# Kernel optimization log

Hardware: AMD Instinct MI355X
Metric: run time of the kernel (lower is better)

Reference implementation:

```python
import jax, jax.numpy as jnp
import numpy as np
import math

H_HEADS, N_LEVELS, N_POINTS, DIM = 8, 4, 4, 256
HEAD_DIM = DIM // H_HEADS
SHAPES = np.array([[150, 150], [75, 75], [38, 38], [19, 19]], dtype=np.int32)
LEVEL_START = np.concatenate([[0], np.cumsum(SHAPES[:, 0] * SHAPES[:, 1])[:-1]]).astype(np.int32)
NUM_VALUE = int((SHAPES[:, 0] * SHAPES[:, 1]).sum())  # 29930
BS, NQ = 4, 22500


def _offset_bias():
    # Deformable-DETR init: points arranged on rays per head
    thetas = np.arange(H_HEADS, dtype=np.float32) * (2.0 * math.pi / H_HEADS)
    grid = np.stack([np.cos(thetas), np.sin(thetas)], -1)
    grid = grid / np.abs(grid).max(-1, keepdims=True)
    grid = np.tile(grid[:, None, None, :], (1, N_LEVELS, N_POINTS, 1))
    grid = grid * (np.arange(N_POINTS, dtype=np.float32) + 1.0)[None, None, :, None]
    return jnp.asarray(grid.reshape(-1))


def setup_inputs() -> dict:
    key = jax.random.key(0)
    ks = jax.random.split(key, 8)
    xav = lambda k, fi, fo: jax.random.normal(k, (fi, fo), jnp.float32) * np.float32(math.sqrt(2.0 / (fi + fo)))
    return {
        "query": jax.random.normal(ks[0], (BS, NQ, DIM), jnp.float32),
        "value": jax.random.normal(ks[1], (BS, NUM_VALUE, DIM), jnp.float32),
        "reference_points": jax.random.uniform(ks[2], (BS, NQ, N_LEVELS, 2), jnp.float32),
        "spatial_shapes": jnp.asarray(SHAPES),
        "level_start_index": jnp.asarray(LEVEL_START),
        "W_so": xav(ks[3], DIM, H_HEADS * N_LEVELS * N_POINTS * 2) * 0.1,
        "b_so": _offset_bias(),
        "W_aw": xav(ks[4], DIM, H_HEADS * N_LEVELS * N_POINTS) * 0.1,
        "b_aw": jnp.zeros((H_HEADS * N_LEVELS * N_POINTS,), jnp.float32),
        "W_v": xav(ks[5], DIM, DIM),
        "b_v": jnp.zeros((DIM,), jnp.float32),
        "W_o": xav(ks[6], DIM, DIM),
        "b_o": jnp.zeros((DIM,), jnp.float32),
    }


def _sample_level(v_l, loc_l, h, w):
    # v_l: (bs, H, h*w, hd); loc_l: (bs, nq, H, P, 2) in [0,1] normalized coords
    # torch grid_sample bilinear, align_corners=False, padding_mode='zeros'
    bs, nq = loc_l.shape[0], loc_l.shape[1]
    x = jnp.transpose(loc_l[..., 0], (0, 2, 1, 3)).reshape(bs, H_HEADS, nq * N_POINTS) * w - 0.5
    y = jnp.transpose(loc_l[..., 1], (0, 2, 1, 3)).reshape(bs, H_HEADS, nq * N_POINTS) * h - 0.5
    x0 = jnp.floor(x); y0 = jnp.floor(y)
    lx = x - x0; ly = y - y0

    def gather(xi, yi, wgt):
        valid = ((xi >= 0) & (xi < w) & (yi >= 0) & (yi < h)).astype(v_l.dtype)
        idx = (jnp.clip(yi, 0, h - 1) * w + jnp.clip(xi, 0, w - 1)).astype(jnp.int32)
        g = jnp.take_along_axis(v_l, idx[..., None], axis=2)  # (bs,H,nq*P,hd)
        return g * (wgt * valid)[..., None]

    x0i = x0.astype(jnp.int32); y0i = y0.astype(jnp.int32)
    out = (gather(x0i, y0i, (1 - lx) * (1 - ly))
           + gather(x0i + 1, y0i, lx * (1 - ly))
           + gather(x0i, y0i + 1, (1 - lx) * ly)
           + gather(x0i + 1, y0i + 1, lx * ly))
    return out.reshape(bs, H_HEADS, nq, N_POINTS, HEAD_DIM)


def reference(query, value, reference_points, spatial_shapes, level_start_index,
              W_so, b_so, W_aw, b_aw, W_v, b_v, W_o, b_o):
    shapes = np.asarray(jax.device_get(spatial_shapes))  # static level shapes
    starts = np.asarray(jax.device_get(level_start_index))
    bs, nq, _ = query.shape
    nv = value.shape[1]

    v = (value @ W_v + b_v).reshape(bs, nv, H_HEADS, HEAD_DIM)
    v = jnp.transpose(v, (0, 2, 1, 3))  # (bs, H, nv, hd)

    off = (query @ W_so + b_so).reshape(bs, nq, H_HEADS, N_LEVELS, N_POINTS, 2)
    aw = jax.nn.softmax((query @ W_aw + b_aw).reshape(bs, nq, H_HEADS, N_LEVELS * N_POINTS), axis=-1)
    aw = aw.reshape(bs, nq, H_HEADS, N_LEVELS, N_POINTS)

    norm = jnp.asarray(np.stack([shapes[:, 1], shapes[:, 0]], -1), query.dtype)  # (L, 2) = (W, H)
    loc = reference_points[:, :, None, :, None, :] + off / norm[None, None, None, :, None, :]

    res = jnp.zeros((bs, nq, H_HEADS, HEAD_DIM), query.dtype)
    for lvl in range(N_LEVELS):
        h, w = int(shapes[lvl, 0]), int(shapes[lvl, 1])
        s = int(starts[lvl])
        v_l = v[:, :, s:s + h * w, :]
        sampled = _sample_level(v_l, loc[:, :, :, lvl], h, w)  # (bs,H,nq,P,hd)
        res = res + jnp.einsum('bhqpd,bqhp->bqhd', sampled, aw[:, :, :, lvl])

    out = res.reshape(bs, nq, DIM) @ W_o + b_o
    return out  # dropout is identity in eval mode
```

## Files before the change

### kernel.cpp

```cpp
#include <hip/hip_runtime.h>
#include <hip/hip_bf16.h>

#define HH 8
#define NL 4
#define NP 4
#define DDIM 256
#define HD 32
#define BSZ 4
#define NQQ 22500
#define NVV 29930

typedef __attribute__((ext_vector_type(4))) float f32x4;
typedef __attribute__((ext_vector_type(8))) short s16x8;

__device__ __forceinline__ float bf16bits2float(unsigned short u) {
    union { unsigned int i; float f; } x;
    x.i = ((unsigned int)u) << 16;
    return x.f;
}
__device__ __forceinline__ unsigned short bfb(float x) {
    union { float f; unsigned int i; } u; u.f = x;
    unsigned int lsb = (u.i >> 16) & 1u;
    u.i += 0x7fffu + lsb;
    return (unsigned short)(u.i >> 16);
}
__device__ __forceinline__ s16x8 cvt8(float4 a, float4 b) {
    s16x8 r;
    r[0] = (short)bfb(a.x); r[1] = (short)bfb(a.y);
    r[2] = (short)bfb(a.z); r[3] = (short)bfb(a.w);
    r[4] = (short)bfb(b.x); r[5] = (short)bfb(b.y);
    r[6] = (short)bfb(b.z); r[7] = (short)bfb(b.w);
    return r;
}

__global__ __launch_bounds__(64) void k_pack(
    const float* __restrict__ Wso, const float* __restrict__ Waw,
    const float* __restrict__ Wv,  const float* __restrict__ Wo,
    unsigned short* __restrict__ pWv, unsigned short* __restrict__ pQP,
    unsigned short* __restrict__ pWo)
{
    const int ctg = blockIdx.x;
    const int lane = threadIdx.x;
    const float* src; unsigned short* dst; int N, col, ct;
    if (ctg < 16)      { ct = ctg;      dst = pWv; src = Wv; N = 256; col = ct*16 + (lane&15); }
    else if (ctg < 40) { ct = ctg - 16; dst = pQP;
        if (ct < 16) { src = Wso; N = 256; col = ct*16 + (lane&15); }
        else         { src = Waw; N = 128; col = (ct-16)*16 + (lane&15); } }
    else               { ct = ctg - 40; dst = pWo; src = Wo; N = 256; col = ct*16 + (lane&15); }

    for (int ks = 0; ks < 8; ++ks) {
        const int k0 = ks*32 + (lane>>4)*8;
        unsigned short tmp[8];
#pragma unroll
        for (int i = 0; i < 8; ++i) tmp[i] = bfb(src[(size_t)(k0 + i) * N + col]);
        unsigned short* d = dst + ((size_t)(ct*8 + ks)*64 + lane)*8;
#pragma unroll
        for (int i = 0; i < 8; ++i) d[i] = tmp[i];
    }
}

__global__ __launch_bounds__(256) void k_value_proj(
    const float* __restrict__ value,
    const float* __restrict__ bv,
    const unsigned short* __restrict__ pWv,
    unsigned short* __restrict__ vout)
{
    const int tid = threadIdx.x;
    const int b   = blockIdx.y;
    const int row0 = blockIdx.x * 64;
    const int w = tid >> 6, lane = tid & 63;
    const int mrow = lane & 15, kg = lane >> 4;

    const int rowa = row0 + w*16 + mrow;
    const bool rv = rowa < NVV;
    const float* ap = value + ((size_t)b * NVV + (rv ? rowa : 0)) * DDIM + kg*8;

    s16x8 af[8];
#pragma unroll
    for (int ks = 0; ks < 8; ++ks) {
        float4 a0 = make_float4(0.f,0.f,0.f,0.f), a1 = a0;
        if (rv) { a0 = *(const float4*)(ap + ks*32); a1 = *(const float4*)(ap + ks*32 + 4); }
        af[ks] = cvt8(a0, a1);
    }
    const s16x8* bp = (const s16x8*)pWv;
#pragma unroll 2
    for (int ct = 0; ct < 16; ++ct) {
        const float bias = bv[ct*16 + mrow];
        f32x4 acc = {bias, bias, bias, bias};
#pragma unroll
        for (int ks = 0; ks < 8; ++ks)
            acc = __builtin_amdgcn_mfma_f32_16x16x32_bf16(af[ks], bp[(ct*8 + ks)*64 + lane], acc, 0, 0, 0);
        const int h = ct >> 1, d = (ct & 1)*16 + mrow;
        unsigned short* vp = vout + ((size_t)(b*HH + h) * NVV) * HD + d;
#pragma unroll
        for (int r = 0; r < 4; ++r) {
            const int rowd = row0 + w*16 + kg*4 + r;
            if (rowd < NVV) vp[(size_t)rowd * HD] = bfb(acc[r]);
        }
    }
}

__global__ __launch_bounds__(256, 5) void k_query_fused(
    const float* __restrict__ query,
    const float* __restrict__ refpt,
    const unsigned short* __restrict__ pQP,
    const unsigned short* __restrict__ pWo,
    const float* __restrict__ bso, const float* __restrict__ baw,
    const float* __restrict__ bo,
    const unsigned short* __restrict__ v,
    float* __restrict__ out)
{
    __shared__ __align__(16) unsigned char s_a8[16 * 512];
    __shared__ float s_so[16 * 256];
    __shared__ float s_aw[16 * 128];

    const int tid = threadIdx.x;
    const int b   = blockIdx.y;
    const int q0  = blockIdx.x * 16;
    const int w = tid >> 6, lane = tid & 63;
    const int mrow = lane & 15, kg = lane >> 4;

    {
        const int r  = tid >> 4;
        const int c0 = (tid & 15) * 16;
        const bool rv = (q0 + r) < NQQ;
        const float* qrow = query + ((size_t)b * NQQ + q0 + r) * DDIM + c0;
        float4 a0 = make_float4(0,0,0,0), a1 = a0, a2 = a0, a3 = a0;
        if (rv) { a0 = *(const float4*)(qrow); a1 = *(const float4*)(qrow+4);
                  a2 = *(const float4*)(qrow+8); a3 = *(const float4*)(qrow+12); }
        const int base = r*512 + c0*2;
        const int sw = (r & 7) << 4;
        *(s16x8*)(s_a8 + ((base     ) ^ sw)) = cvt8(a0, a1);
        *(s16x8*)(s_a8 + ((base + 16) ^ sw)) = cvt8(a2, a3);
    }
    __syncthreads();

    {
        s16x8 af[8];
        const int sw = (mrow & 7) << 4;
#pragma unroll
        for (int ks = 0; ks < 8; ++ks)
            af[ks] = *(const s16x8*)(s_a8 + ((mrow*512 + (ks*32 + kg*8)*2) ^ sw));
        const s16x8* bq = (const s16x8*)pQP;
#pragma unroll
        for (int t = 0; t < 6; ++t) {
            const int ct = w*6 + t;
            const float bias = (ct < 16) ? bso[ct*16 + mrow] : baw[(ct-16)*16 + mrow];
            f32x4 acc = {bias, bias, bias, bias};
#pragma unroll
            for (int ks = 0; ks < 8; ++ks)
                acc = __builtin_amdgcn_mfma_f32_16x16x32_bf16(af[ks], bq[(ct*8 + ks)*64 + lane], acc, 0, 0, 0);
            if (ct < 16) {
#pragma unroll
                for (int r = 0; r < 4; ++r) s_so[(kg*4 + r)*256 + ct*16 + mrow] = acc[r];
            } else {
#pragma unroll
                for (int r = 0; r < 4; ++r) s_aw[(kg*4 + r)*128 + (ct-16)*16 + mrow] = acc[r];
            }
        }
    }
    __syncthreads();

    if (tid < 128) {
        const int q = tid >> 3, h = tid & 7;
        float* p = s_aw + q * 128 + h * 16;
        float m = p[0];
#pragma unroll
        for (int i = 1; i < 16; ++i) m = fmaxf(m, p[i]);
        float e[16], s = 0.f;
#pragma unroll
        for (int i = 0; i < 16; ++i) { e[i] = __expf(p[i] - m); s += e[i]; }
        const float inv = 1.f / s;
#pragma unroll
        for (int i = 0; i < 16; ++i) p[i] = e[i] * inv;
    }
    __syncthreads();

    {
        const int lane8 = tid & 7;
        const int d4 = lane8 * 4;
        const int g = tid >> 3;
        const int hs[4]   = {150, 75, 38, 19};
        const int strt[4] = {0, 22500, 28125, 29569};
#pragma unroll
        for (int it = 0; it < 4; ++it) {
            const int pair = g + 32 * it;
            const int q = pair >> 3, h = pair & 7;
            float4 acc = make_float4(0.f, 0.f, 0.f, 0.f);
            if (q0 + q < NQQ) {
                const float* rp = refpt + ((size_t)b * NQQ + q0 + q) * (NL * 2);
                const unsigned short* vb = v + ((size_t)(b * HH + h) * NVV) * HD + d4;
                const float* soq = s_so + q * 256 + h * 32;
                const float* awq = s_aw + q * 128 + h * 16;
#pragma unroll
                for (int l = 0; l < NL; ++l) {
                    const int hl = hs[l];
                    const int wl = hl;
                    const float invwh = 1.f / (float)hl;
                    const float rx = rp[l * 2 + 0];
                    const float ry = rp[l * 2 + 1];
                    const unsigned short* vl = vb + (size_t)strt[l] * HD;
#pragma unroll
                    for (int p = 0; p < NP; ++p) {
                        const float ox = soq[(l * NP + p) * 2 + 0];
                        const float oy = soq[(l * NP + p) * 2 + 1];
                        const float awv = awq[l * NP + p];
                        const float x = fmaf(ox, invwh, rx) * (float)wl - 0.5f;
                        const float y = fmaf(oy, invwh, ry) * (float)hl - 0.5f;
                        const float xf = floorf(x), yf = floorf(y);
                        const float lx = x - xf, ly = y - yf;
                        const int x0 = (int)xf, y0 = (int)yf;
                        const int x1 = x0 + 1, y1 = y0 + 1;
                        const int cx0 = min(max(x0, 0), wl - 1);
                        const int cx1 = min(max(x1, 0), wl - 1);
                        const int cy0 = min(max(y0, 0), hl - 1);
                        const int cy1 = min(max(y1, 0), hl - 1);
                        const float vx0 = (x0 >= 0 && x0 < wl) ? 1.f : 0.f;
                        const float vx1 = (x1 >= 0 && x1 < wl) ? 1.f : 0.f;
                        const float vy0 = (y0 >= 0 && y0 < hl) ? 1.f : 0.f;
                        const float vy1 = (y1 >= 0 && y1 < hl) ? 1.f : 0.f;
                        const float w00 = awv * (1.f - lx) * (1.f - ly) * vx0 * vy0;
                        const float w10 = awv * lx * (1.f - ly) * vx1 * vy0;
                        const float w01 = awv * (1.f - lx) * ly * vx0 * vy1;
                        const float w11 = awv * lx * ly * vx1 * vy1;
                        const ushort4 s00 = *(const ushort4*)(vl + (size_t)(cy0 * wl + cx0) * HD);
                        const ushort4 s10 = *(const ushort4*)(vl + (size_t)(cy0 * wl + cx1) * HD);
                        const ushort4 s01 = *(const ushort4*)(vl + (size_t)(cy1 * wl + cx0) * HD);
                        const ushort4 s11 = *(const ushort4*)(vl + (size_t)(cy1 * wl + cx1) * HD);
                        acc.x = fmaf(w00, bf16bits2float(s00.x), acc.x);
                        acc.y = fmaf(w00, bf16bits2float(s00.y), acc.y);
                        acc.z = fmaf(w00, bf16bits2float(s00.z), acc.z);
                        acc.w = fmaf(w00, bf16bits2float(s00.w), acc.w);
                        acc.x = fmaf(w10, bf16bits2float(s10.x), acc.x);
                        acc.y = fmaf(w10, bf16bits2float(s10.y), acc.y);
                        acc.z = fmaf(w10, bf16bits2float(s10.z), acc.z);
                        acc.w = fmaf(w10, bf16bits2float(s10.w), acc.w);
                        acc.x = fmaf(w01, bf16bits2float(s01.x), acc.x);
                        acc.y = fmaf(w01, bf16bits2float(s01.y), acc.y);
                        acc.z = fmaf(w01, bf16bits2float(s01.z), acc.z);
                        acc.w = fmaf(w01, bf16bits2float(s01.w), acc.w);
                        acc.x = fmaf(w11, bf16bits2float(s11.x), acc.x);
                        acc.y = fmaf(w11, bf16bits2float(s11.y), acc.y);
                        acc.z = fmaf(w11, bf16bits2float(s11.z), acc.z);
                        acc.w = fmaf(w11, bf16bits2float(s11.w), acc.w);
                    }
                }
            }
            ushort4 rb;
            rb.x = bfb(acc.x); rb.y = bfb(acc.y); rb.z = bfb(acc.z); rb.w = bfb(acc.w);
            const int boff = q*512 + (h*32 + d4)*2;
            *(ushort4*)(s_a8 + (boff ^ ((q & 7) << 4))) = rb;
        }
    }
    __syncthreads();

    {
        s16x8 of[8];
        const int sw = (mrow & 7) << 4;
#pragma unroll
        for (int ks = 0; ks < 8; ++ks)
            of[ks] = *(const s16x8*)(s_a8 + ((mrow*512 + (ks*32 + kg*8)*2) ^ sw));
        const s16x8* bp = (const s16x8*)pWo;
#pragma unroll
        for (int t = 0; t < 4; ++t) {
            const int ct = w*4 + t;
            const float bias = bo[ct*16 + mrow];
            f32x4 acc = {bias, bias, bias, bias};
#pragma unroll
            for (int ks = 0; ks < 8; ++ks)
                acc = __builtin_amdgcn_mfma_f32_16x16x32_bf16(of[ks], bp[(ct*8 + ks)*64 + lane], acc, 0, 0, 0);
#pragma unroll
            for (int r = 0; r < 4; ++r) {
                const int q = kg*4 + r;
                if (q0 + q < NQQ)
                    out[((size_t)b * NQQ + q0 + q) * DDIM + ct*16 + mrow] = acc[r];
            }
        }
    }
}

extern "C" void kernel_launch(void* const* d_in, const int* in_sizes, int n_in,
                              void* d_out, int out_size, void* d_ws, size_t ws_size,
                              hipStream_t stream) {
    const float* query = (const float*)d_in[0];
    const float* value = (const float*)d_in[1];
    const float* refpt = (const float*)d_in[2];
    const float* Wso = (const float*)d_in[5];
    const float* bso = (const float*)d_in[6];
    const float* Waw = (const float*)d_in[7];
    const float* baw = (const float*)d_in[8];
    const float* Wv  = (const float*)d_in[9];
    const float* bv  = (const float*)d_in[10];
    const float* Wo  = (const float*)d_in[11];
    const float* bo  = (const float*)d_in[12];
    float* out = (float*)d_out;

    unsigned short* v   = (unsigned short*)d_ws;
    unsigned short* pWv = (unsigned short*)((char*)d_ws + 61296640);
    unsigned short* pQP = pWv + 65536;
    unsigned short* pWo = pQP + 98304;

    k_pack<<<56, 64, 0, stream>>>(Wso, Waw, Wv, Wo, pWv, pQP, pWo);

    dim3 g1((NVV + 63) / 64, BSZ);
    k_value_proj<<<g1, 256, 0, stream>>>(value, bv, pWv, v);

    dim3 g2((NQQ + 15) / 16, BSZ);
    k_query_fused<<<g2, 256, 0, stream>>>(query, refpt, pQP, pWo, bso, baw, bo, v, out);
}
```

Before: 421.6 us.

## Remap deformable sampling to per-wave heads with 16-byte gathers and packed FMA

Restructures the bilinear sampling stage so each wave handles one head, with 16 queries times 4 groups of 8 channels. Each corner is gathered as a 16-byte load and accumulated with v_pk_fma_f32. The offset and attention-weight shared buffers are transposed to head-major layout so this mapping reads them with per-query strides, and the softmax indexing is adjusted to match. It also swaps software bf16 rounding for the hardware v_cvt_pk_bf16_f32 instruction and adds nontemporal loads for query/value and stores for the output. The aim is fewer, wider gather instructions and cheaper conversions, at the cost of more live registers per thread and possible LDS bank-conflict changes.

```diff
diff --git a/kernel.cpp b/kernel.cpp
--- a/kernel.cpp
+++ b/kernel.cpp
@@ -11,12 +11,19 @@
 #define NVV 29930
 
 typedef __attribute__((ext_vector_type(4))) float f32x4;
+typedef __attribute__((ext_vector_type(2))) float f32x2;
 typedef __attribute__((ext_vector_type(8))) short s16x8;
-
-__device__ __forceinline__ float bf16bits2float(unsigned short u) {
-    union { unsigned int i; float f; } x;
-    x.i = ((unsigned int)u) << 16;
-    return x.f;
+typedef __attribute__((ext_vector_type(4))) unsigned int u32x4;
+
+__device__ __forceinline__ unsigned int cvtpk(float lo, float hi) {
+    unsigned int r;
+    asm("v_cvt_pk_bf16_f32 %0, %1, %2" : "=v"(r) : "v"(lo), "v"(hi));
+    return r;
+}
+__device__ __forceinline__ unsigned int cvtpk1(float lo) {
+    unsigned int r;
+    asm("v_cvt_pk_bf16_f32 %0, %1, 0" : "=v"(r) : "v"(lo));
+    return r;
 }
 __device__ __forceinline__ unsigned short bfb(float x) {
     union { float f; unsigned int i; } u; u.f = x;
@@ -24,13 +31,16 @@
     u.i += 0x7fffu + lsb;
     return (unsigned short)(u.i >> 16);
 }
-__device__ __forceinline__ s16x8 cvt8(float4 a, float4 b) {
-    s16x8 r;
-    r[0] = (short)bfb(a.x); r[1] = (short)bfb(a.y);
-    r[2] = (short)bfb(a.z); r[3] = (short)bfb(a.w);
-    r[4] = (short)bfb(b.x); r[5] = (short)bfb(b.y);
-    r[6] = (short)bfb(b.z); r[7] = (short)bfb(b.w);
-    return r;
+__device__ __forceinline__ s16x8 cvt8(f32x4 a, f32x4 b) {
+    union { unsigned int u[4]; s16x8 v; } r;
+    r.u[0] = cvtpk(a[0], a[1]);
+    r.u[1] = cvtpk(a[2], a[3]);
+    r.u[2] = cvtpk(b[0], b[1]);
+    r.u[3] = cvtpk(b[2], b[3]);
+    return r.v;
+}
+__device__ __forceinline__ void pk_fma(f32x2& a, f32x2 v, f32x2 w) {
+    asm("v_pk_fma_f32 %0, %1, %2, %0" : "+v"(a) : "v"(v), "v"(w));
 }
 
 __global__ __launch_bounds__(64) void k_pack(
@@ -78,8 +88,11 @@
     s16x8 af[8];
 #pragma unroll
     for (int ks = 0; ks < 8; ++ks) {
-        float4 a0 = make_float4(0.f,0.f,0.f,0.f), a1 = a0;
-        if (rv) { a0 = *(const float4*)(ap + ks*32); a1 = *(const float4*)(ap + ks*32 + 4); }
+        f32x4 a0 = {0.f,0.f,0.f,0.f}, a1 = a0;
+        if (rv) {
+            a0 = __builtin_nontemporal_load((const f32x4*)(ap + ks*32));
+            a1 = __builtin_nontemporal_load((const f32x4*)(ap + ks*32 + 4));
+        }
         af[ks] = cvt8(a0, a1);
     }
     const s16x8* bp = (const s16x8*)pWv;
@@ -95,7 +108,7 @@
 #pragma unroll
         for (int r = 0; r < 4; ++r) {
             const int rowd = row0 + w*16 + kg*4 + r;
-            if (rowd < NVV) vp[(size_t)rowd * HD] = bfb(acc[r]);
+            if (rowd < NVV) vp[(size_t)rowd * HD] = (unsigned short)cvtpk1(acc[r]);
         }
     }
 }
@@ -111,8 +124,8 @@
     float* __restrict__ out)
 {
     __shared__ __align__(16) unsigned char s_a8[16 * 512];
-    __shared__ float s_so[16 * 256];
-    __shared__ float s_aw[16 * 128];
+    __shared__ float s_so[8 * 512];
+    __shared__ float s_aw[8 * 256];
 
     const int tid = threadIdx.x;
     const int b   = blockIdx.y;
@@ -125,9 +138,13 @@
         const int c0 = (tid & 15) * 16;
         const bool rv = (q0 + r) < NQQ;
         const float* qrow = query + ((size_t)b * NQQ + q0 + r) * DDIM + c0;
-        float4 a0 = make_float4(0,0,0,0), a1 = a0, a2 = a0, a3 = a0;
-        if (rv) { a0 = *(const float4*)(qrow); a1 = *(const float4*)(qrow+4);
-                  a2 = *(const float4*)(qrow+8); a3 = *(const float4*)(qrow+12); }
+        f32x4 a0 = {0,0,0,0}, a1 = a0, a2 = a0, a3 = a0;
+        if (rv) {
+            a0 = __builtin_nontemporal_load((const f32x4*)(qrow));
+            a1 = __builtin_nontemporal_load((const f32x4*)(qrow+4));
+            a2 = __builtin_nontemporal_load((const f32x4*)(qrow+8));
+            a3 = __builtin_nontemporal_load((const f32x4*)(qrow+12));
+        }
         const int base = r*512 + c0*2;
         const int sw = (r & 7) << 4;
         *(s16x8*)(s_a8 + ((base     ) ^ sw)) = cvt8(a0, a1);
@@ -137,10 +154,10 @@
 
     {
         s16x8 af[8];
-        const int sw = (mrow & 7) << 4;
+        const int swz = (mrow & 7) << 4;
 #pragma unroll
         for (int ks = 0; ks < 8; ++ks)
-            af[ks] = *(const s16x8*)(s_a8 + ((mrow*512 + (ks*32 + kg*8)*2) ^ sw));
+            af[ks] = *(const s16x8*)(s_a8 + ((mrow*512 + (ks*32 + kg*8)*2) ^ swz));
         const s16x8* bq = (const s16x8*)pQP;
 #pragma unroll
         for (int t = 0; t < 6; ++t) {
@@ -151,11 +168,15 @@
             for (int ks = 0; ks < 8; ++ks)
                 acc = __builtin_amdgcn_mfma_f32_16x16x32_bf16(af[ks], bq[(ct*8 + ks)*64 + lane], acc, 0, 0, 0);
             if (ct < 16) {
-#pragma unroll
-                for (int r = 0; r < 4; ++r) s_so[(kg*4 + r)*256 + ct*16 + mrow] = acc[r];
+                const int c = ct*16 + mrow;
+                float* d = s_so + (c >> 5)*512 + (c & 31)*16 + kg*4;
+#pragma unroll
+                for (int r = 0; r < 4; ++r) d[r] = acc[r];
             } else {
-#pragma unroll
-                for (int r = 0; r < 4; ++r) s_aw[(kg*4 + r)*128 + (ct-16)*16 + mrow] = acc[r];
+                const int c = (ct-16)*16 + mrow;
+                float* d = s_aw + (c >> 4)*256 + (c & 15)*16 + kg*4;
+#pragma unroll
+                for (int r = 0; r < 4; ++r) d[r] = acc[r];
             }
         }
     }
@@ -163,103 +184,100 @@
 
     if (tid < 128) {
         const int q = tid >> 3, h = tid & 7;
-        float* p = s_aw + q * 128 + h * 16;
+        float* p = s_aw + h * 256 + q;
         float m = p[0];
 #pragma unroll
-        for (int i = 1; i < 16; ++i) m = fmaxf(m, p[i]);
+        for (int i = 1; i < 16; ++i) m = fmaxf(m, p[i*16]);
         float e[16], s = 0.f;
 #pragma unroll
-        for (int i = 0; i < 16; ++i) { e[i] = __expf(p[i] - m); s += e[i]; }
+        for (int i = 0; i < 16; ++i) { e[i] = __expf(p[i*16] - m); s += e[i]; }
         const float inv = 1.f / s;
 #pragma unroll
-        for (int i = 0; i < 16; ++i) p[i] = e[i] * inv;
+        for (int i = 0; i < 16; ++i) p[i*16] = e[i] * inv;
     }
     __syncthreads();
 
     {
-        const int lane8 = tid & 7;
-        const int d4 = lane8 * 4;
-        const int g = tid >> 3;
-        const int hs[4]   = {150, 75, 38, 19};
-        const int strt[4] = {0, 22500, 28125, 29569};
-#pragma unroll
-        for (int it = 0; it < 4; ++it) {
-            const int pair = g + 32 * it;
-            const int q = pair >> 3, h = pair & 7;
-            float4 acc = make_float4(0.f, 0.f, 0.f, 0.f);
-            if (q0 + q < NQQ) {
-                const float* rp = refpt + ((size_t)b * NQQ + q0 + q) * (NL * 2);
-                const unsigned short* vb = v + ((size_t)(b * HH + h) * NVV) * HD + d4;
-                const float* soq = s_so + q * 256 + h * 32;
-                const float* awq = s_aw + q * 128 + h * 16;
-#pragma unroll
-                for (int l = 0; l < NL; ++l) {
-                    const int hl = hs[l];
-                    const int wl = hl;
-                    const float invwh = 1.f / (float)hl;
-                    const float rx = rp[l * 2 + 0];
-                    const float ry = rp[l * 2 + 1];
-                    const unsigned short* vl = vb + (size_t)strt[l] * HD;
-#pragma unroll
-                    for (int p = 0; p < NP; ++p) {
-                        const float ox = soq[(l * NP + p) * 2 + 0];
-                        const float oy = soq[(l * NP + p) * 2 + 1];
-                        const float awv = awq[l * NP + p];
-                        const float x = fmaf(ox, invwh, rx) * (float)wl - 0.5f;
-                        const float y = fmaf(oy, invwh, ry) * (float)hl - 0.5f;
-                        const float xf = floorf(x), yf = floorf(y);
-                        const float lx = x - xf, ly = y - yf;
-                        const int x0 = (int)xf, y0 = (int)yf;
-                        const int x1 = x0 + 1, y1 = y0 + 1;
-                        const int cx0 = min(max(x0, 0), wl - 1);
-                        const int cx1 = min(max(x1, 0), wl - 1);
-                        const int cy0 = min(max(y0, 0), hl - 1);
-                        const int cy1 = min(max(y1, 0), hl - 1);
-                        const float vx0 = (x0 >= 0 && x0 < wl) ? 1.f : 0.f;
-                        const float vx1 = (x1 >= 0 && x1 < wl) ? 1.f : 0.f;
-                        const float vy0 = (y0 >= 0 && y0 < hl) ? 1.f : 0.f;
-                        const float vy1 = (y1 >= 0 && y1 < hl) ? 1.f : 0.f;
-                        const float w00 = awv * (1.f - lx) * (1.f - ly) * vx0 * vy0;
-                        const float w10 = awv * lx * (1.f - ly) * vx1 * vy0;
-                        const float w01 = awv * (1.f - lx) * ly * vx0 * vy1;
-                        const float w11 = awv * lx * ly * vx1 * vy1;
-                        const ushort4 s00 = *(const ushort4*)(vl + (size_t)(cy0 * wl + cx0) * HD);
-                        const ushort4 s10 = *(const ushort4*)(vl + (size_t)(cy0 * wl + cx1) * HD);
-                        const ushort4 s01 = *(const ushort4*)(vl + (size_t)(cy1 * wl + cx0) * HD);
-                        const ushort4 s11 = *(const ushort4*)(vl + (size_t)(cy1 * wl + cx1) * HD);
-                        acc.x = fmaf(w00, bf16bits2float(s00.x), acc.x);
-                        acc.y = fmaf(w00, bf16bits2float(s00.y), acc.y);
-                        acc.z = fmaf(w00, bf16bits2float(s00.z), acc.z);
-                        acc.w = fmaf(w00, bf16bits2float(s00.w), acc.w);
-                        acc.x = fmaf(w10, bf16bits2float(s10.x), acc.x);
-                        acc.y = fmaf(w10, bf16bits2float(s10.y), acc.y);
-                        acc.z = fmaf(w10, bf16bits2float(s10.z), acc.z);
-                        acc.w = fmaf(w10, bf16bits2float(s10.w), acc.w);
-                        acc.x = fmaf(w01, bf16bits2float(s01.x), acc.x);
-                        acc.y = fmaf(w01, bf16bits2float(s01.y), acc.y);
-                        acc.z = fmaf(w01, bf16bits2float(s01.z), acc.z);
-                        acc.w = fmaf(w01, bf16bits2float(s01.w), acc.w);
-                        acc.x = fmaf(w11, bf16bits2float(s11.x), acc.x);
-                        acc.y = fmaf(w11, bf16bits2float(s11.y), acc.y);
-                        acc.z = fmaf(w11, bf16bits2float(s11.z), acc.z);
-                        acc.w = fmaf(w11, bf16bits2float(s11.w), acc.w);
-                    }
+        const int qs = lane >> 2;
+        const int dg = lane & 3;
+        const int qv = (q0 + qs < NQQ) ? (q0 + qs) : (NQQ - 1);
+        const float2* rp2 = (const float2*)(refpt + ((size_t)b * NQQ + qv) * (NL * 2));
+#pragma unroll
+        for (int pass = 0; pass < 2; ++pass) {
+            const int h = __builtin_amdgcn_readfirstlane(pass * 4 + w);
+            const unsigned short* vbh = v + ((size_t)(b*HH + h) * NVV) * HD + dg*8;
+            const float* soh = s_so + h * 512 + qs;
+            const float* awh = s_aw + h * 256 + qs;
+            f32x2 acc0 = {0.f,0.f}, acc1 = {0.f,0.f}, acc2 = {0.f,0.f}, acc3 = {0.f,0.f};
+            const int hs_[4] = {150, 75, 38, 19};
+            const int st_[4] = {0, 22500, 28125, 29569};
+#pragma unroll
+            for (int l = 0; l < NL; ++l) {
+                const int L = hs_[l];
+                const float Lf = (float)L;
+                const float2 rxy = rp2[l];
+                const unsigned short* vlp = vbh + (size_t)st_[l] * HD;
+#pragma unroll
+                for (int p = 0; p < NP; ++p) {
+                    const int lp = l*4 + p;
+                    const float ox  = soh[(2*lp    ) * 16];
+                    const float oy  = soh[(2*lp + 1) * 16];
+                    const float awv = awh[lp * 16];
+                    const float x = fmaf(rxy.x, Lf, ox) - 0.5f;
+                    const float y = fmaf(rxy.y, Lf, oy) - 0.5f;
+                    const float xf = floorf(x), yf = floorf(y);
+                    const float lx = x - xf, ly = y - yf;
+                    const int x0 = (int)xf, y0 = (int)yf;
+                    const int x1 = x0 + 1, y1 = y0 + 1;
+                    const int cx0 = min(max(x0, 0), L-1), cx1 = min(max(x1, 0), L-1);
+                    const int cy0 = min(max(y0, 0), L-1), cy1 = min(max(y1, 0), L-1);
+                    const bool bx0 = (unsigned)x0 < (unsigned)L;
+                    const bool bx1 = (unsigned)x1 < (unsigned)L;
+                    const bool by0 = (unsigned)y0 < (unsigned)L;
+                    const bool by1 = (unsigned)y1 < (unsigned)L;
+                    const unsigned r0 = (unsigned)(cy0 * L), r1 = (unsigned)(cy1 * L);
+                    const u32x4 c00 = *(const u32x4*)(vlp + (size_t)((r0 + cx0) * HD));
+                    const u32x4 c10 = *(const u32x4*)(vlp + (size_t)((r0 + cx1) * HD));
+                    const u32x4 c01 = *(const u32x4*)(vlp + (size_t)((r1 + cx0) * HD));
+                    const u32x4 c11 = *(const u32x4*)(vlp + (size_t)((r1 + cx1) * HD));
+                    const float t1 = awv * ly, t0 = awv - t1;
+                    const float lxc = 1.f - lx;
+                    const float w00 = (bx0 & by0) ? lxc * t0 : 0.f;
+                    const float w10 = (bx1 & by0) ? lx  * t0 : 0.f;
+                    const float w01 = (bx0 & by1) ? lxc * t1 : 0.f;
+                    const float w11 = (bx1 & by1) ? lx  * t1 : 0.f;
+#define CORNER(cv, wgt) { \
+    f32x2 ww = {wgt, wgt}; \
+    f32x2 v0 = {__uint_as_float((cv)[0] << 16), __uint_as_float((cv)[0] & 0xffff0000u)}; \
+    f32x2 v1 = {__uint_as_float((cv)[1] << 16), __uint_as_float((cv)[1] & 0xffff0000u)}; \
+    f32x2 v2 = {__uint_as_float((cv)[2] << 16), __uint_as_float((cv)[2] & 0xffff0000u)}; \
+    f32x2 v3 = {__uint_as_float((cv)[3] << 16), __uint_as_float((cv)[3] & 0xffff0000u)}; \
+    pk_fma(acc0, v0, ww); pk_fma(acc1, v1, ww); \
+    pk_fma(acc2, v2, ww); pk_fma(acc3, v3, ww); }
+                    CORNER(c00, w00)
+                    CORNER(c10, w10)
+                    CORNER(c01, w01)
+                    CORNER(c11, w11)
+#undef CORNER
                 }
             }
-            ushort4 rb;
-            rb.x = bfb(acc.x); rb.y = bfb(acc.y); rb.z = bfb(acc.z); rb.w = bfb(acc.w);
-            const int boff = q*512 + (h*32 + d4)*2;
-            *(ushort4*)(s_a8 + (boff ^ ((q & 7) << 4))) = rb;
+            u32x4 rb;
+            rb[0] = cvtpk(acc0[0], acc0[1]);
+            rb[1] = cvtpk(acc1[0], acc1[1]);
+            rb[2] = cvtpk(acc2[0], acc2[1]);
+            rb[3] = cvtpk(acc3[0], acc3[1]);
+            const int boff = qs*512 + (h*32 + dg*8)*2;
+            *(u32x4*)(s_a8 + (boff ^ ((qs & 7) << 4))) = rb;
         }
     }
     __syncthreads();
 
     {
         s16x8 of[8];
-        const int sw = (mrow & 7) << 4;
+        const int swz = (mrow & 7) << 4;
 #pragma unroll
         for (int ks = 0; ks < 8; ++ks)
-            of[ks] = *(const s16x8*)(s_a8 + ((mrow*512 + (ks*32 + kg*8)*2) ^ sw));
+            of[ks] = *(const s16x8*)(s_a8 + ((mrow*512 + (ks*32 + kg*8)*2) ^ swz));
         const s16x8* bp = (const s16x8*)pWo;
 #pragma unroll
         for (int t = 0; t < 4; ++t) {
@@ -273,7 +291,8 @@
             for (int r = 0; r < 4; ++r) {
                 const int q = kg*4 + r;
                 if (q0 + q < NQQ)
-                    out[((size_t)b * NQQ + q0 + q) * DDIM + ct*16 + mrow] = acc[r];
+                    __builtin_nontemporal_store(acc[r],
+                        &out[((size_t)b * NQQ + q0 + q) * DDIM + ct*16 + mrow]);
             }
         }
     }
```

New measurement: 353.3 us. -16.2%, faster.
